# Performance work log

Measured on AMD Instinct MI355X. Metric: run time of the kernel, lower is better.

Reference implementation:

```python
import jax, jax.numpy as jnp
import numpy as np

N_NODES = 50000
N_EDGES = 800000
IN_NODE = 256
IN_EDGE = 64
OUT_DIM = 128


def setup_inputs() -> dict:
    key = jax.random.key(0)
    k1, k2, k3, k4, k5, k6, k7 = jax.random.split(key, 7)
    feats_node = jax.random.normal(k1, (N_NODES, IN_NODE), dtype=jnp.float32)
    feats_edge = jax.random.normal(k2, (N_EDGES, IN_EDGE), dtype=jnp.float32)
    src = jax.random.randint(k3, (N_EDGES,), 0, N_NODES, dtype=jnp.int32)
    dst = jax.random.randint(k4, (N_EDGES,), 0, N_NODES, dtype=jnp.int32)
    # weights init: normal(std=0.5), torch Linear stores [out, in]
    Wn = 0.5 * jax.random.normal(k5, (OUT_DIM, IN_NODE), dtype=jnp.float32)
    We = 0.5 * jax.random.normal(k6, (IN_EDGE, IN_EDGE), dtype=jnp.float32)
    Wa = 0.5 * jax.random.normal(k7, (1, 2 * OUT_DIM + IN_EDGE), dtype=jnp.float32)
    return {"feats_node": feats_node, "feats_edge": feats_edge,
            "src": src, "dst": dst, "Wn": Wn, "We": We, "Wa": Wa}


def reference(feats_node, feats_edge, src, dst, Wn, We, Wa):
    n_nodes = feats_node.shape[0]
    # node / edge projections
    z = feats_node @ Wn.T            # [N, out_dim]
    ze = feats_edge @ We.T           # [E, in_dim_edge]
    # per-edge attention logit: attn_fc(cat(z_src, z_dst, z_edge)) + leaky_relu
    z3 = jnp.concatenate([z[src], z[dst], ze], axis=1)   # [E, 2*out+edge]
    a = z3 @ Wa.T                                        # [E, 1]
    e = jax.nn.leaky_relu(a, negative_slope=0.2)[:, 0]   # [E]
    # segment softmax over incoming edges of each dst node (numerically stable)
    m = jax.ops.segment_max(e, dst, num_segments=n_nodes)        # [N]
    m = jnp.where(jnp.isfinite(m), m, 0.0)                       # isolated nodes
    e_exp = jnp.exp(e - m[dst])                                  # [E]
    denom = jax.ops.segment_sum(e_exp, dst, num_segments=n_nodes)  # [N]
    alpha = e_exp / jnp.maximum(denom[dst], 1e-38)               # [E]
    # weighted scatter-sum of source messages
    h = jax.ops.segment_sum(alpha[:, None] * z[src], dst, num_segments=n_nodes)
    return h, ze
```

## Files before the change

kernel.cpp:

```cpp
#include <hip/hip_runtime.h>
#include <hip/hip_bf16.h>
#include <math.h>

#define N_NODES 50000
#define N_EDGES 800000
#define IN_NODE 256
#define IN_EDGE 64
#define OUT_DIM 128

typedef __attribute__((ext_vector_type(8))) short short8;
typedef __attribute__((ext_vector_type(4))) float f32x4;

__device__ inline short f2bf(float x) {
    union { float f; unsigned u; } v; v.f = x;
    unsigned r = v.u + 0x7fff + ((v.u >> 16) & 1);
    return (short)(r >> 16);
}

__device__ inline void cvt_store8(short* p, float4 a, float4 b) {
    union { short h[8]; uint4 u; } t;
    t.h[0] = f2bf(a.x); t.h[1] = f2bf(a.y); t.h[2] = f2bf(a.z); t.h[3] = f2bf(a.w);
    t.h[4] = f2bf(b.x); t.h[5] = f2bf(b.y); t.h[6] = f2bf(b.z); t.h[7] = f2bf(b.w);
    *(uint4*)p = t.u;
}

__global__ void k0_ve(const float* __restrict__ We, const float* __restrict__ Wa,
                      float* __restrict__ v_e)
{
    const int k = threadIdx.x;
    if (k < IN_EDGE) {
        float s = 0.f;
        for (int c = 0; c < IN_EDGE; ++c)
            s += We[c * IN_EDGE + k] * Wa[2 * OUT_DIM + c];
        v_e[k] = s;
    }
}

__global__ __launch_bounds__(256) void k_deg(const int* __restrict__ dst,
                                             int* __restrict__ deg)
{
    const int i = (blockIdx.x * 256 + threadIdx.x) * 4;
    if (i < N_EDGES) {
        const int4 d = *(const int4*)&dst[i];
        atomicAdd(&deg[d.x], 1);
        atomicAdd(&deg[d.y], 1);
        atomicAdd(&deg[d.z], 1);
        atomicAdd(&deg[d.w], 1);
    }
}

#define K1_MT 64
#define K1_KT 32

__global__ __launch_bounds__(256) void k1_node_gemm(
    const float* __restrict__ fn, const float* __restrict__ Wn,
    const float* __restrict__ Wa,
    __hip_bfloat16* __restrict__ zb,
    float* __restrict__ s_src, float* __restrict__ s_dst)
{
    __shared__ float A_s[K1_KT][K1_MT + 4];
    __shared__ float B_s[K1_KT][OUT_DIM + 4];
    __shared__ float red_s[K1_MT][17];
    __shared__ float red_d[K1_MT][17];

    const int t  = threadIdx.x;
    const int m0 = blockIdx.x * K1_MT;
    const int tn = t & 15;
    const int tm = t >> 4;
    const int r0 = tm * 4;
    const int c0 = tn * 8;

    float acc[4][8];
    for (int i = 0; i < 4; ++i)
        for (int j = 0; j < 8; ++j) acc[i][j] = 0.f;

    for (int k0 = 0; k0 < IN_NODE; k0 += K1_KT) {
        {
            const int chunk = t & 7;
            const int nd    = t >> 3;
            for (int hh = 0; hh < 2; ++hh) {
                const int node = nd + hh * 32;
                int gr = m0 + node; if (gr >= N_NODES) gr = N_NODES - 1;
                const float4 v = *(const float4*)&fn[(size_t)gr * IN_NODE + k0 + chunk * 4];
                A_s[chunk * 4 + 0][node] = v.x;
                A_s[chunk * 4 + 1][node] = v.y;
                A_s[chunk * 4 + 2][node] = v.z;
                A_s[chunk * 4 + 3][node] = v.w;
            }
        }
        {
            const int chunk = t & 7;
            const int cb    = t >> 3;
            for (int hh = 0; hh < 4; ++hh) {
                const int c = cb + hh * 32;
                const float4 v = *(const float4*)&Wn[(size_t)c * IN_NODE + k0 + chunk * 4];
                B_s[chunk * 4 + 0][c] = v.x;
                B_s[chunk * 4 + 1][c] = v.y;
                B_s[chunk * 4 + 2][c] = v.z;
                B_s[chunk * 4 + 3][c] = v.w;
            }
        }
        __syncthreads();

        for (int k = 0; k < K1_KT; ++k) {
            const float4 a  = *(const float4*)&A_s[k][r0];
            const float4 b0 = *(const float4*)&B_s[k][c0];
            const float4 b1 = *(const float4*)&B_s[k][c0 + 4];
            const float av[4] = {a.x, a.y, a.z, a.w};
            const float bv[8] = {b0.x, b0.y, b0.z, b0.w, b1.x, b1.y, b1.z, b1.w};
            for (int i = 0; i < 4; ++i)
                for (int j = 0; j < 8; ++j)
                    acc[i][j] += av[i] * bv[j];
        }
        __syncthreads();
    }

    float wa_s[8], wa_d[8];
    for (int j = 0; j < 8; ++j) {
        wa_s[j] = Wa[c0 + j];
        wa_d[j] = Wa[OUT_DIM + c0 + j];
    }
    float ps[4], pd[4];
    for (int i = 0; i < 4; ++i) {
        float a = 0.f, b = 0.f;
        for (int j = 0; j < 8; ++j) {
            a += wa_s[j] * acc[i][j];
            b += wa_d[j] * acc[i][j];
        }
        ps[i] = a; pd[i] = b;
    }

    for (int i = 0; i < 4; ++i) {
        const int node = m0 + r0 + i;
        if (node < N_NODES) {
            alignas(16) __hip_bfloat16 tmp[8];
            for (int j = 0; j < 8; ++j) tmp[j] = __float2bfloat16(acc[i][j]);
            *(uint4*)&zb[(size_t)node * OUT_DIM + c0] = *(const uint4*)tmp;
        }
    }

    for (int i = 0; i < 4; ++i) {
        red_s[r0 + i][tn] = ps[i];
        red_d[r0 + i][tn] = pd[i];
    }
    __syncthreads();
    if (t < K1_MT) {
        const int node = m0 + t;
        if (node < N_NODES) {
            float a = 0.f, b = 0.f;
            for (int j = 0; j < 16; ++j) { a += red_s[t][j]; b += red_d[t][j]; }
            s_src[node] = a;
            s_dst[node] = b;
        }
    }
}

__global__ __launch_bounds__(256) void k2_edge_gemm_mfma(
    const float* __restrict__ fe, const float* __restrict__ We,
    const float* __restrict__ v_e,
    const int* __restrict__ src, const int* __restrict__ dst,
    const float* __restrict__ s_src, const float* __restrict__ s_dst,
    int* __restrict__ cursor,
    float* __restrict__ ze_out, int* __restrict__ csr_src,
    float* __restrict__ csr_e)
{
    __shared__ alignas(16) short A_lds[128][72];
    __shared__ alignas(16) short B_lds[64][72];
    __shared__ float se_lds[128];

    const int t    = threadIdx.x;
    const int lane = t & 63;
    const int w    = t >> 6;
    const long e0  = (long)blockIdx.x * 128;

    {
        const int edge = t >> 1, half = t & 1;
        const float4* rp = (const float4*)&fe[(e0 + edge) * IN_EDGE + half * 32];
        float4 va[8];
        for (int q = 0; q < 8; ++q) va[q] = rp[q];

        float part = 0.f;
        for (int q = 0; q < 8; ++q) {
            const float4 w4 = *(const float4*)&v_e[half * 32 + q * 4];
            part += va[q].x * w4.x + va[q].y * w4.y
                  + va[q].z * w4.z + va[q].w * w4.w;
        }
        const float other = __shfl_xor(part, 1, 64);
        if (half == 0) se_lds[edge] = part + other;

        short* wp = &A_lds[edge][half * 32];
        for (int q = 0; q < 4; ++q)
            cvt_store8(wp + q * 8, va[2 * q], va[2 * q + 1]);
    }
    {
        const int row = t >> 2, kq = (t & 3) * 16;
        const float4* rp = (const float4*)&We[(size_t)row * IN_EDGE + kq];
        cvt_store8(&B_lds[row][kq + 0], rp[0], rp[1]);
        cvt_store8(&B_lds[row][kq + 8], rp[2], rp[3]);
    }
    __syncthreads();

    const int lrow = lane & 15;
    const int lk   = (lane >> 4) * 8;

    f32x4 acc[2][4];
    for (int r = 0; r < 2; ++r)
        for (int c = 0; c < 4; ++c)
            acc[r][c] = (f32x4){0.f, 0.f, 0.f, 0.f};

    for (int s = 0; s < 2; ++s) {
        const int kk = s * 32 + lk;
        short8 aF[2], bF[4];
        for (int r = 0; r < 2; ++r)
            aF[r] = *(const short8*)&A_lds[w * 32 + r * 16 + lrow][kk];
        for (int c = 0; c < 4; ++c)
            bF[c] = *(const short8*)&B_lds[c * 16 + lrow][kk];
        for (int r = 0; r < 2; ++r)
            for (int c = 0; c < 4; ++c)
                acc[r][c] = __builtin_amdgcn_mfma_f32_16x16x32_bf16(
                    aF[r], bF[c], acc[r][c], 0, 0, 0);
    }

    const int rquad = lane >> 4;
    for (int r = 0; r < 2; ++r) {
        for (int c = 0; c < 4; ++c) {
            for (int reg = 0; reg < 4; ++reg) {
                const long row = e0 + w * 32 + r * 16 + rquad * 4 + reg;
                ze_out[row * IN_EDGE + c * 16 + lrow] = acc[r][c][reg];
            }
        }
    }

    if (t < 128) {
        const long e = e0 + t;
        const int d = dst[e];
        const int s = src[e];
        float lg = s_src[s] + s_dst[d] + se_lds[t];
        lg = (lg > 0.f) ? lg : 0.2f * lg;
        const int pos = atomicAdd(&cursor[d], 1);
        csr_src[pos] = s;
        csr_e[pos]   = lg;
    }
}

#define SCAN_T 1024
#define SCAN_C 49

__global__ __launch_bounds__(SCAN_T) void k4_scan(
    const int* __restrict__ deg, int* __restrict__ off, int* __restrict__ cursor)
{
    __shared__ int part[SCAN_T];
    const int t = threadIdx.x;
    const int lo = t * SCAN_C;
    int hi = lo + SCAN_C; if (hi > N_NODES) hi = N_NODES;

    int s = 0;
    for (int i = lo; i < hi; ++i) s += deg[i];
    part[t] = s;
    __syncthreads();
    for (int d = 1; d < SCAN_T; d <<= 1) {
        int v = 0;
        if (t >= d) v = part[t - d];
        __syncthreads();
        if (t >= d) part[t] += v;
        __syncthreads();
    }
    int run = (t == 0) ? 0 : part[t - 1];
    for (int i = lo; i < hi; ++i) {
        off[i] = run; cursor[i] = run;
        run += deg[i];
    }
    if (t == SCAN_T - 1) off[N_NODES] = part[SCAN_T - 1];
}

__global__ __launch_bounds__(256) void k6_aggregate(
    const int* __restrict__ off, const int* __restrict__ csr_src,
    const float* __restrict__ csr_e, const __hip_bfloat16* __restrict__ zb,
    float* __restrict__ h)
{
    const int node = (int)((blockIdx.x * blockDim.x + threadIdx.x) >> 6);
    const int lane = threadIdx.x & 63;
    if (node >= N_NODES) return;

    const int beg = off[node];
    const int end = off[node + 1];
    const int deg = end - beg;

    const int cgrp = lane & 15;
    const int eidx = lane >> 4;

    float out[8] = {0.f, 0.f, 0.f, 0.f, 0.f, 0.f, 0.f, 0.f};

    if (deg > 0) {
        float m = -INFINITY;
        for (int j = lane; j < deg; j += 64) m = fmaxf(m, csr_e[beg + j]);
        for (int o = 32; o > 0; o >>= 1) m = fmaxf(m, __shfl_xor(m, o, 64));

        float l = 0.f;
        for (int c0 = 0; c0 < deg; c0 += 64) {
            const int cl = min(64, deg - c0);
            float wv = 0.f;
            if (lane < cl) wv = __expf(csr_e[beg + c0 + lane] - m);
            float ws = wv;
            for (int o = 32; o > 0; o >>= 1) ws += __shfl_xor(ws, o, 64);
            l += ws;

            for (int jj = 0; jj < cl; jj += 4) {
                const int j  = jj + eidx;
                const int jc = (j < cl) ? j : (cl - 1);
                const float wgt = __shfl(wv, jc, 64);
                if (j < cl) {
                    const int s = csr_src[beg + c0 + j];
                    const uint4 zv = *(const uint4*)&zb[(size_t)s * OUT_DIM + cgrp * 8];
                    const unsigned* zu = (const unsigned*)&zv;
                    for (int q = 0; q < 4; ++q) {
                        out[2 * q]     += wgt * __uint_as_float(zu[q] << 16);
                        out[2 * q + 1] += wgt * __uint_as_float(zu[q] & 0xffff0000u);
                    }
                }
            }
        }
        for (int i = 0; i < 8; ++i) {
            out[i] += __shfl_xor(out[i], 16, 64);
            out[i] += __shfl_xor(out[i], 32, 64);
        }
        const float inv = 1.f / fmaxf(l, 1e-38f);
        for (int i = 0; i < 8; ++i) out[i] *= inv;
    }

    if (lane < 16) {
        float4 o0 = make_float4(out[0], out[1], out[2], out[3]);
        float4 o1 = make_float4(out[4], out[5], out[6], out[7]);
        float* hp = &h[(size_t)node * OUT_DIM + lane * 8];
        *(float4*)(hp + 0) = o0;
        *(float4*)(hp + 4) = o1;
    }
}

extern "C" void kernel_launch(void* const* d_in, const int* in_sizes, int n_in,
                              void* d_out, int out_size, void* d_ws, size_t ws_size,
                              hipStream_t stream)
{
    const float* fn  = (const float*)d_in[0];
    const float* fe  = (const float*)d_in[1];
    const int*   src = (const int*)d_in[2];
    const int*   dst = (const int*)d_in[3];
    const float* Wn  = (const float*)d_in[4];
    const float* We  = (const float*)d_in[5];
    const float* Wa  = (const float*)d_in[6];

    float* h_out  = (float*)d_out;
    float* ze_out = h_out + (size_t)N_NODES * OUT_DIM;

    char* p = (char*)d_ws;
    auto alloc = [&](size_t bytes) -> char* {
        char* r = p;
        p += (bytes + 255) & ~(size_t)255;
        return r;
    };
    __hip_bfloat16* zb = (__hip_bfloat16*)alloc((size_t)N_NODES * OUT_DIM * 2);
    float* s_src   = (float*)alloc((size_t)N_NODES * 4);
    float* s_dst   = (float*)alloc((size_t)N_NODES * 4);
    int*   deg     = (int*)alloc((size_t)N_NODES * 4);
    int*   off     = (int*)alloc((size_t)(N_NODES + 1) * 4);
    int*   cursor  = (int*)alloc((size_t)N_NODES * 4);
    int*   csr_src = (int*)alloc((size_t)N_EDGES * 4);
    float* csr_e   = (float*)alloc((size_t)N_EDGES * 4);
    float* v_e     = (float*)alloc((size_t)IN_EDGE * 4);

    hipMemsetAsync(deg, 0, (size_t)N_NODES * sizeof(int), stream);

    k0_ve<<<1, 64, 0, stream>>>(We, Wa, v_e);
    k_deg<<<(N_EDGES / 4 + 255) / 256, 256, 0, stream>>>(dst, deg);
    k4_scan<<<1, SCAN_T, 0, stream>>>(deg, off, cursor);
    k1_node_gemm<<<(N_NODES + K1_MT - 1) / K1_MT, 256, 0, stream>>>(
        fn, Wn, Wa, zb, s_src, s_dst);
    k2_edge_gemm_mfma<<<N_EDGES / 128, 256, 0, stream>>>(
        fe, We, v_e, src, dst, s_src, s_dst, cursor, ze_out, csr_src, csr_e);
    k6_aggregate<<<(N_NODES + 3) / 4, 256, 0, stream>>>(
        off, csr_src, csr_e, zb, h_out);
}
```

Baseline: 686.6 us.

## Move node GEMM to bf16 MFMA and fold attention weights into input-space vectors

Replaces the FP32 scalar-FMA node projection with a bf16 MFMA 16x16x32 tiled kernel over 128-node tiles. The attention scores s_src/s_dst are no longer reduced from the projected z. They are computed as dot products of the raw fp32 node features with precomputed vectors u = Wn^T·Wa, which a prep kernel now builds. This removes the LDS reduction and the FP32 FMA bottleneck of the old GEMM. The cost is bf16 rounding of inputs in z, plus uncoalesced scalar bf16 stores of the output.

```diff
diff --git a/kernel.cpp b/kernel.cpp
--- a/kernel.cpp
+++ b/kernel.cpp
@@ -24,8 +24,10 @@
     *(uint4*)p = t.u;
 }
 
-__global__ void k0_ve(const float* __restrict__ We, const float* __restrict__ Wa,
-                      float* __restrict__ v_e)
+__global__ __launch_bounds__(256) void k0_prep(
+    const float* __restrict__ We, const float* __restrict__ Wn,
+    const float* __restrict__ Wa,
+    float* __restrict__ v_e, float* __restrict__ u_src, float* __restrict__ u_dst)
 {
     const int k = threadIdx.x;
     if (k < IN_EDGE) {
@@ -34,6 +36,14 @@
             s += We[c * IN_EDGE + k] * Wa[2 * OUT_DIM + c];
         v_e[k] = s;
     }
+    float a = 0.f, b = 0.f;
+    for (int c = 0; c < OUT_DIM; ++c) {
+        const float w = Wn[(size_t)c * IN_NODE + k];
+        a += Wa[c] * w;
+        b += Wa[OUT_DIM + c] * w;
+    }
+    u_src[k] = a;
+    u_dst[k] = b;
 }
 
 __global__ __launch_bounds__(256) void k_deg(const int* __restrict__ dst,
@@ -49,108 +59,97 @@
     }
 }
 
-#define K1_MT 64
-#define K1_KT 32
-
-__global__ __launch_bounds__(256) void k1_node_gemm(
+#define K1_BK 64
+
+__global__ __launch_bounds__(256) void k1_node_mfma(
     const float* __restrict__ fn, const float* __restrict__ Wn,
-    const float* __restrict__ Wa,
+    const float* __restrict__ u_src, const float* __restrict__ u_dst,
     __hip_bfloat16* __restrict__ zb,
     float* __restrict__ s_src, float* __restrict__ s_dst)
 {
-    __shared__ float A_s[K1_KT][K1_MT + 4];
-    __shared__ float B_s[K1_KT][OUT_DIM + 4];
-    __shared__ float red_s[K1_MT][17];
-    __shared__ float red_d[K1_MT][17];
-
-    const int t  = threadIdx.x;
-    const int m0 = blockIdx.x * K1_MT;
-    const int tn = t & 15;
-    const int tm = t >> 4;
-    const int r0 = tm * 4;
-    const int c0 = tn * 8;
-
-    float acc[4][8];
-    for (int i = 0; i < 4; ++i)
-        for (int j = 0; j < 8; ++j) acc[i][j] = 0.f;
-
-    for (int k0 = 0; k0 < IN_NODE; k0 += K1_KT) {
+    __shared__ alignas(16) short A_lds[128][72];
+    __shared__ alignas(16) short B_lds[128][72];
+
+    const int t    = threadIdx.x;
+    const int lane = t & 63;
+    const int w    = t >> 6;
+    const int m0   = blockIdx.x * 128;
+
+    const int nd   = t >> 1;
+    const int half = t & 1;
+
+    int grow = m0 + nd; if (grow >= N_NODES) grow = N_NODES - 1;
+    const float* arow = &fn[(size_t)grow * IN_NODE];
+    const float* brow = &Wn[(size_t)nd * IN_NODE];
+
+    float sa = 0.f, sb = 0.f;
+
+    const int lrow = lane & 15;
+    const int lk   = (lane >> 4) * 8;
+
+    f32x4 acc[2][8];
+    for (int r = 0; r < 2; ++r)
+        for (int c = 0; c < 8; ++c)
+            acc[r][c] = (f32x4){0.f, 0.f, 0.f, 0.f};
+
+    for (int k0 = 0; k0 < IN_NODE; k0 += K1_BK) {
         {
-            const int chunk = t & 7;
-            const int nd    = t >> 3;
-            for (int hh = 0; hh < 2; ++hh) {
-                const int node = nd + hh * 32;
-                int gr = m0 + node; if (gr >= N_NODES) gr = N_NODES - 1;
-                const float4 v = *(const float4*)&fn[(size_t)gr * IN_NODE + k0 + chunk * 4];
-                A_s[chunk * 4 + 0][node] = v.x;
-                A_s[chunk * 4 + 1][node] = v.y;
-                A_s[chunk * 4 + 2][node] = v.z;
-                A_s[chunk * 4 + 3][node] = v.w;
+            const float4* rp = (const float4*)&arow[k0 + half * 32];
+            float4 va[8];
+            for (int q = 0; q < 8; ++q) va[q] = rp[q];
+            for (int q = 0; q < 8; ++q) {
+                const float4 us = *(const float4*)&u_src[k0 + half * 32 + q * 4];
+                const float4 ud = *(const float4*)&u_dst[k0 + half * 32 + q * 4];
+                sa += va[q].x * us.x + va[q].y * us.y + va[q].z * us.z + va[q].w * us.w;
+                sb += va[q].x * ud.x + va[q].y * ud.y + va[q].z * ud.z + va[q].w * ud.w;
             }
+            short* wp = &A_lds[nd][half * 32];
+            for (int q = 0; q < 4; ++q)
+                cvt_store8(wp + q * 8, va[2 * q], va[2 * q + 1]);
         }
         {
-            const int chunk = t & 7;
-            const int cb    = t >> 3;
-            for (int hh = 0; hh < 4; ++hh) {
-                const int c = cb + hh * 32;
-                const float4 v = *(const float4*)&Wn[(size_t)c * IN_NODE + k0 + chunk * 4];
-                B_s[chunk * 4 + 0][c] = v.x;
-                B_s[chunk * 4 + 1][c] = v.y;
-                B_s[chunk * 4 + 2][c] = v.z;
-                B_s[chunk * 4 + 3][c] = v.w;
+            const float4* rp = (const float4*)&brow[k0 + half * 32];
+            float4 vb[8];
+            for (int q = 0; q < 8; ++q) vb[q] = rp[q];
+            short* wp = &B_lds[nd][half * 32];
+            for (int q = 0; q < 4; ++q)
+                cvt_store8(wp + q * 8, vb[2 * q], vb[2 * q + 1]);
+        }
+        __syncthreads();
+
+        for (int s = 0; s < 2; ++s) {
+            const int kk = s * 32 + lk;
+            short8 aF[2], bF[8];
+            for (int r = 0; r < 2; ++r)
+                aF[r] = *(const short8*)&A_lds[w * 32 + r * 16 + lrow][kk];
+            for (int c = 0; c < 8; ++c)
+                bF[c] = *(const short8*)&B_lds[c * 16 + lrow][kk];
+            for (int r = 0; r < 2; ++r)
+                for (int c = 0; c < 8; ++c)
+                    acc[r][c] = __builtin_amdgcn_mfma_f32_16x16x32_bf16(
+                        aF[r], bF[c], acc[r][c], 0, 0, 0);
+        }
+        __syncthreads();
+    }
+
+    {
+        const float oa = __shfl_xor(sa, 1, 64);
+        const float ob = __shfl_xor(sb, 1, 64);
+        if (half == 0 && (m0 + nd) < N_NODES) {
+            s_src[m0 + nd] = sa + oa;
+            s_dst[m0 + nd] = sb + ob;
+        }
+    }
+
+    const int rq = lane >> 4;
+    for (int r = 0; r < 2; ++r) {
+        for (int reg = 0; reg < 4; ++reg) {
+            const int row = m0 + w * 32 + r * 16 + rq * 4 + reg;
+            if (row < N_NODES) {
+                for (int c = 0; c < 8; ++c)
+                    zb[(size_t)row * OUT_DIM + c * 16 + lrow] =
+                        __float2bfloat16(acc[r][c][reg]);
             }
-        }
-        __syncthreads();
-
-        for (int k = 0; k < K1_KT; ++k) {
-            const float4 a  = *(const float4*)&A_s[k][r0];
-            const float4 b0 = *(const float4*)&B_s[k][c0];
-            const float4 b1 = *(const float4*)&B_s[k][c0 + 4];
-            const float av[4] = {a.x, a.y, a.z, a.w};
-            const float bv[8] = {b0.x, b0.y, b0.z, b0.w, b1.x, b1.y, b1.z, b1.w};
-            for (int i = 0; i < 4; ++i)
-                for (int j = 0; j < 8; ++j)
-                    acc[i][j] += av[i] * bv[j];
-        }
-        __syncthreads();
-    }
-
-    float wa_s[8], wa_d[8];
-    for (int j = 0; j < 8; ++j) {
-        wa_s[j] = Wa[c0 + j];
-        wa_d[j] = Wa[OUT_DIM + c0 + j];
-    }
-    float ps[4], pd[4];
-    for (int i = 0; i < 4; ++i) {
-        float a = 0.f, b = 0.f;
-        for (int j = 0; j < 8; ++j) {
-            a += wa_s[j] * acc[i][j];
-            b += wa_d[j] * acc[i][j];
-        }
-        ps[i] = a; pd[i] = b;
-    }
-
-    for (int i = 0; i < 4; ++i) {
-        const int node = m0 + r0 + i;
-        if (node < N_NODES) {
-            alignas(16) __hip_bfloat16 tmp[8];
-            for (int j = 0; j < 8; ++j) tmp[j] = __float2bfloat16(acc[i][j]);
-            *(uint4*)&zb[(size_t)node * OUT_DIM + c0] = *(const uint4*)tmp;
-        }
-    }
-
-    for (int i = 0; i < 4; ++i) {
-        red_s[r0 + i][tn] = ps[i];
-        red_d[r0 + i][tn] = pd[i];
-    }
-    __syncthreads();
-    if (t < K1_MT) {
-        const int node = m0 + t;
-        if (node < N_NODES) {
-            float a = 0.f, b = 0.f;
-            for (int j = 0; j < 16; ++j) { a += red_s[t][j]; b += red_d[t][j]; }
-            s_src[node] = a;
-            s_dst[node] = b;
         }
     }
 }
@@ -367,14 +366,16 @@
     int*   csr_src = (int*)alloc((size_t)N_EDGES * 4);
     float* csr_e   = (float*)alloc((size_t)N_EDGES * 4);
     float* v_e     = (float*)alloc((size_t)IN_EDGE * 4);
+    float* u_src   = (float*)alloc((size_t)IN_NODE * 4);
+    float* u_dst   = (float*)alloc((size_t)IN_NODE * 4);
 
     hipMemsetAsync(deg, 0, (size_t)N_NODES * sizeof(int), stream);
 
-    k0_ve<<<1, 64, 0, stream>>>(We, Wa, v_e);
+    k0_prep<<<1, 256, 0, stream>>>(We, Wn, Wa, v_e, u_src, u_dst);
     k_deg<<<(N_EDGES / 4 + 255) / 256, 256, 0, stream>>>(dst, deg);
     k4_scan<<<1, SCAN_T, 0, stream>>>(deg, off, cursor);
-    k1_node_gemm<<<(N_NODES + K1_MT - 1) / K1_MT, 256, 0, stream>>>(
-        fn, Wn, Wa, zb, s_src, s_dst);
+    k1_node_mfma<<<(N_NODES + 127) / 128, 256, 0, stream>>>(
+        fn, Wn, u_src, u_dst, zb, s_src, s_dst);
     k2_edge_gemm_mfma<<<N_EDGES / 128, 256, 0, stream>>>(
         fe, We, v_e, src, dst, s_src, s_dst, cursor, ze_out, csr_src, csr_e);
     k6_aggregate<<<(N_NODES + 3) / 4, 256, 0, stream>>>(
```

After: 664.4 us. 3.2% less time.
